# Kernel optimization log

Measured on AMD Instinct MI355X. Metric: run time of the kernel, lower is better.

The kernel has to match this reference:

```python
import jax, jax.numpy as jnp
import numpy as np
from jax import lax

BN_EPS = 1e-5
HEADS = 2


def dw_conv(x, w, stride, pad):
    # depthwise conv, NCHW, weight OIHW with I=1, groups=C
    return lax.conv_general_dilated(
        x, w, (stride, stride), [(pad, pad), (pad, pad)],
        dimension_numbers=('NCHW', 'OIHW', 'NCHW'),
        feature_group_count=x.shape[1])


def bn(x, g, b, m, v):
    inv = g * lax.rsqrt(v + BN_EPS)
    return (x - m[:, None, None]) * inv[:, None, None] + b[:, None, None]


def conv1x1(x, w, b):
    return jnp.einsum('bchw,oc->bohw', x, w) + b[:, None, None]


def setup_inputs() -> dict:
    key = jax.random.key(0)
    ks = jax.random.split(key, 20)
    B, C, H, W = 32, 128, 56, 56
    r = lambda i, shape, s=0.05: jax.random.normal(ks[i], shape, jnp.float32) * s
    return {
        'x': jax.random.normal(ks[0], (B, C, H, W), jnp.float32),
        'q_w': r(1, (C, C)), 'q_b': r(2, (C,)),
        'kv_w': r(3, (2 * C, C)), 'kv_b': r(4, (2 * C,)),
        'sr1_w': r(5, (C, 1, 4, 4), 0.2),
        'sr1_g': jax.random.uniform(ks[6], (C,), jnp.float32) + 0.5,
        'sr1_b': r(7, (C,)),
        'sr1_m': r(8, (C,)),
        'sr1_v': jax.random.uniform(ks[9], (C,), jnp.float32) + 0.5,
        'sr2_w': r(10, (C, 1, 1, 1), 0.5),
        'sr2_g': jax.random.uniform(ks[11], (C,), jnp.float32) + 0.5,
        'sr2_b': r(12, (C,)),
        'sr2_m': r(13, (C,)),
        'sr2_v': jax.random.uniform(ks[14], (C,), jnp.float32) + 0.5,
        'local_w': r(15, (C, 1, 3, 3), 0.2), 'local_b': r(16, (C,)),
    }


def reference(x, q_w, q_b, kv_w, kv_b,
              sr1_w, sr1_g, sr1_b, sr1_m, sr1_v,
              sr2_w, sr2_g, sr2_b, sr2_m, sr2_v,
              local_w, local_b):
    B, C, H, W = x.shape
    h = HEADS
    d = C // h
    scale = d ** -0.5

    # q projection: 1x1 conv -> [B, h, N, d]
    q = conv1x1(x, q_w, q_b)
    q = q.reshape(B, h, d, H * W).transpose(0, 1, 3, 2)

    # spatial reduction: depthwise strided conv + BN + ReLU, then depthwise 1x1 + BN
    kv = jax.nn.relu(bn(dw_conv(x, sr1_w, 4, 2), sr1_g, sr1_b, sr1_m, sr1_v))
    kv = bn(kv * sr2_w.reshape(C, 1, 1), sr2_g, sr2_b, sr2_m, sr2_v)

    # depthwise 3x3 local conv + residual
    kv = dw_conv(kv, local_w, 1, 1) + local_b[:, None, None] + kv

    # kv projection and split
    kvp = conv1x1(kv, kv_w, kv_b)
    k, v = jnp.split(kvp, 2, axis=1)
    Nk = k.shape[2] * k.shape[3]
    k = k.reshape(B, h, d, Nk)                       # [B,h,d,Nk]
    v = v.reshape(B, h, d, Nk).transpose(0, 1, 3, 2)  # [B,h,Nk,d]

    attn = jax.nn.softmax(jnp.einsum('bhnd,bhdm->bhnm', q, k) * scale, axis=-1)
    out = jnp.einsum('bhnm,bhmd->bhnd', attn, v)      # [B,h,N,d]
    return out.transpose(0, 1, 3, 2).reshape(B, C, H, W)
```

## Files before the change

kernel.cpp:

```cpp
#include <hip/hip_runtime.h>
#include <hip/hip_bf16.h>

#define B_    32
#define C_    128
#define H_    56
#define W_    56
#define N_    3136
#define HK_   15
#define NK_   225
#define D_    64

typedef __attribute__((ext_vector_type(8))) short bf16x8;
typedef __attribute__((ext_vector_type(4))) float f32x4;

__device__ __forceinline__ float b2f(unsigned short u) {
    union { float f; unsigned int i; } x;
    x.i = ((unsigned int)u) << 16;
    return x.f;
}
__device__ __forceinline__ unsigned short f2b(float f) {
    __hip_bfloat16 h = __float2bfloat16(f);
    return *(unsigned short*)&h;
}

__device__ __forceinline__ void gll16(const char* g, char* l) {
    __builtin_amdgcn_global_load_lds(
        (const __attribute__((address_space(1))) unsigned int*)g,
        (__attribute__((address_space(3))) unsigned int*)l,
        16, 0, 0);
}

__global__ __launch_bounds__(256) void srlocal_kernel(
        const float* __restrict__ x,
        const float* __restrict__ sr1_w, const float* __restrict__ sr1_g,
        const float* __restrict__ sr1_b, const float* __restrict__ sr1_m,
        const float* __restrict__ sr1_v, const float* __restrict__ sr2_w,
        const float* __restrict__ sr2_g, const float* __restrict__ sr2_b,
        const float* __restrict__ sr2_m, const float* __restrict__ sr2_v,
        const float* __restrict__ local_w, const float* __restrict__ local_b,
        float* __restrict__ kv2) {
    int bc = blockIdx.x;
    int c  = bc & (C_ - 1);
    int tid = threadIdx.x;
    __shared__ float xim[H_ * W_];
    __shared__ float kvt[HK_][HK_ + 1];

    const float* xp = x + (size_t)bc * (H_ * W_);
    for (int idx = tid; idx < (H_ * W_) / 4; idx += 256)
        ((float4*)xim)[idx] = ((const float4*)xp)[idx];
    __syncthreads();

    int p = tid;
    int oy = p / HK_, ox = p % HK_;
    if (p < NK_) {
        float s = 0.f;
#pragma unroll
        for (int ky = 0; ky < 4; ++ky) {
            int iy = oy * 4 - 2 + ky;
            if (iy < 0 || iy >= H_) continue;
#pragma unroll
            for (int kx = 0; kx < 4; ++kx) {
                int ix = ox * 4 - 2 + kx;
                if (ix < 0 || ix >= W_) continue;
                s += xim[iy * W_ + ix] * sr1_w[c * 16 + ky * 4 + kx];
            }
        }
        float inv1 = sr1_g[c] * rsqrtf(sr1_v[c] + 1e-5f);
        s = (s - sr1_m[c]) * inv1 + sr1_b[c];
        s = fmaxf(s, 0.f);
        s *= sr2_w[c];
        float inv2 = sr2_g[c] * rsqrtf(sr2_v[c] + 1e-5f);
        s = (s - sr2_m[c]) * inv2 + sr2_b[c];
        kvt[oy][ox] = s;
    }
    __syncthreads();
    if (p < NK_) {
        float v = kvt[oy][ox] + local_b[c];
#pragma unroll
        for (int dy = -1; dy <= 1; ++dy) {
            int yy = oy + dy;
            if (yy < 0 || yy >= HK_) continue;
#pragma unroll
            for (int dx = -1; dx <= 1; ++dx) {
                int xx = ox + dx;
                if (xx < 0 || xx >= HK_) continue;
                v += kvt[yy][xx] * local_w[c * 9 + (dy + 1) * 3 + (dx + 1)];
            }
        }
        kv2[(size_t)bc * NK_ + p] = v;
    }
}

__global__ __launch_bounds__(256) void wprep_kernel(
        const float* __restrict__ q_w, const float* __restrict__ q_b,
        const float* __restrict__ kv_w, const float* __restrict__ kv_b,
        unsigned short* __restrict__ wkq_sw, unsigned short* __restrict__ wv_sw,
        float* __restrict__ kwb, float* __restrict__ wb, float* __restrict__ qkb) {
    int bx = blockIdx.x;
    int h  = bx >> 3, cg = bx & 7;
    int tid = threadIdx.x;
    __shared__ float wk_s[64][128];
    __shared__ float wq_s[64][16];

    for (int idx = tid; idx < 64 * 128; idx += 256)
        wk_s[idx >> 7][idx & 127] = kv_w[(size_t)(h * 64 + (idx >> 7)) * 128 + (idx & 127)];
    for (int idx = tid; idx < 64 * 16; idx += 256)
        wq_s[idx >> 4][idx & 15] = q_w[(size_t)(h * 64 + (idx >> 4)) * 128 + cg * 16 + (idx & 15)];
    __syncthreads();

    {
        int cl = tid >> 4;
        int c  = cg * 16 + cl;
        int cp0 = (tid & 15) * 8;
        float acc[8];
#pragma unroll
        for (int i = 0; i < 8; ++i) acc[i] = 0.f;
        for (int e = 0; e < 64; ++e) {
            float wqv = wq_s[e][cl];
#pragma unroll
            for (int i = 0; i < 8; ++i) acc[i] += wqv * wk_s[e][cp0 + i];
        }
        char* base = (char*)wkq_sw + (size_t)h * 32768 + (size_t)c * 256;
        ushort4 u0, u1;
        u0.x = f2b(acc[0] * 0.125f); u0.y = f2b(acc[1] * 0.125f);
        u0.z = f2b(acc[2] * 0.125f); u0.w = f2b(acc[3] * 0.125f);
        u1.x = f2b(acc[4] * 0.125f); u1.y = f2b(acc[5] * 0.125f);
        u1.z = f2b(acc[6] * 0.125f); u1.w = f2b(acc[7] * 0.125f);
        int sw = (c & 7) << 4;
        *(ushort4*)(base + ((cp0 * 2) ^ sw)) = u0;
        *(ushort4*)(base + ((cp0 * 2 + 8) ^ sw)) = u1;
    }
    if (tid < 16) {
        int cl = tid, c = cg * 16 + cl;
        float s = 0.f;
        for (int e = 0; e < 64; ++e) s += kv_b[h * 64 + e] * wq_s[e][cl];
        kwb[h * 128 + c] = s * 0.125f;
    }
    if (cg == 0) {
        if (tid < 128) {
            float s = 0.f;
            for (int e = 0; e < 64; ++e) s += q_b[h * 64 + e] * wk_s[e][tid];
            wb[h * 128 + tid] = s * 0.125f;
        }
        if (tid == 0) {
            float s = 0.f;
            for (int e = 0; e < 64; ++e) s += q_b[h * 64 + e] * kv_b[h * 64 + e];
            qkb[h] = s * 0.125f;
        }
    }
    if (cg == 1) {
        for (int idx = tid; idx < 64 * 128; idx += 256) {
            int e = idx >> 7, cp = idx & 127;
            unsigned short val = f2b(kv_w[(size_t)(128 + h * 64 + e) * 128 + cp]);
            *(unsigned short*)((char*)wv_sw + (size_t)h * 16384 + (size_t)e * 256 +
                               (((cp * 2) ^ ((e & 7) << 4)))) = val;
        }
    }
}

#define L2B(r, cb) ((r) * 256 + ((cb) ^ (((r) & 7) << 4)))
__global__ __launch_bounds__(256, 2) void kvw_kernel(
        const float* __restrict__ kv2,
        const float* __restrict__ kv_b,
        const unsigned short* __restrict__ wkq_sw,
        const unsigned short* __restrict__ wv_sw,
        const float* __restrict__ kwb,
        const float* __restrict__ wb,
        const float* __restrict__ qkb,
        unsigned short* __restrict__ kw,
        float* __restrict__ bias_s,
        unsigned short* __restrict__ vbuf) {
    int b = blockIdx.x, h = blockIdx.y, mh = blockIdx.z;
    int bh = b * 2 + h;
    int m0 = mh * 64;
    int tid = threadIdx.x;
    int lo = tid & 15, hi = (tid >> 4) & 3, wid = tid >> 6;

    __shared__ char K2[16384];
    __shared__ char WQ[32768];
    __shared__ char WV[16384];

    {
        const char* srcQ = (const char*)wkq_sw + (size_t)h * 32768 + tid * 16;
        char* dstQ = WQ + wid * 1024;
#pragma unroll
        for (int i = 0; i < 8; ++i) gll16(srcQ + i * 4096, dstQ + i * 4096);
        const char* srcV = (const char*)wv_sw + (size_t)h * 16384 + tid * 16;
        char* dstV = WV + wid * 1024;
#pragma unroll
        for (int i = 0; i < 4; ++i) gll16(srcV + i * 4096, dstV + i * 4096);
    }
    {
        int j = tid & 63;
        int mg = m0 + j;
        bool val = (mg < NK_);
#pragma unroll
        for (int it = 0; it < 8; ++it) {
            int c0 = (tid >> 6) * 4 + it * 16;
            ushort4 u;
            if (val) {
                const float* kp = kv2 + ((size_t)b * 128 + c0) * NK_ + mg;
                u.x = f2b(kp[0]);
                u.y = f2b(kp[NK_]);
                u.z = f2b(kp[2 * NK_]);
                u.w = f2b(kp[3 * NK_]);
            } else { u.x = 0; u.y = 0; u.z = 0; u.w = 0; }
            *(ushort4*)(K2 + L2B(j, c0 * 2)) = u;
        }
    }
    __syncthreads();

    bf16x8 aq[4];
#pragma unroll
    for (int ks = 0; ks < 4; ++ks)
        aq[ks] = *(const bf16x8*)(K2 + L2B(wid * 16 + lo, ks * 64 + hi * 16));

    char* kwB = (char*)kw + (size_t)bh * 65536;
#pragma unroll
    for (int ct = 0; ct < 8; ++ct) {
        f32x4 acc = {0.f, 0.f, 0.f, 0.f};
#pragma unroll
        for (int ks = 0; ks < 4; ++ks) {
            bf16x8 bq = *(const bf16x8*)(WQ + L2B(ct * 16 + lo, ks * 64 + hi * 16));
            acc = __builtin_amdgcn_mfma_f32_16x16x32_bf16(aq[ks], bq, acc, 0, 0, 0);
        }
        int c = ct * 16 + lo;
        float kb = kwb[h * 128 + c];
#pragma unroll
        for (int r = 0; r < 4; ++r) {
            int mg = m0 + wid * 16 + hi * 4 + r;
            *(unsigned short*)(kwB + (size_t)mg * 256 + (((c * 2) ^ ((mg & 7) << 4)))) =
                f2b(acc[r] + kb);
        }
    }

    char* vB = (char*)vbuf + (size_t)bh * 32768;
#pragma unroll
    for (int et = 0; et < 4; ++et) {
        f32x4 acc = {0.f, 0.f, 0.f, 0.f};
#pragma unroll
        for (int ks = 0; ks < 4; ++ks) {
            bf16x8 bv = *(const bf16x8*)(WV + L2B(et * 16 + lo, ks * 64 + hi * 16));
            acc = __builtin_amdgcn_mfma_f32_16x16x32_bf16(aq[ks], bv, acc, 0, 0, 0);
        }
        int e = et * 16 + lo;
        float vb = kv_b[128 + h * 64 + e];
#pragma unroll
        for (int r = 0; r < 4; ++r) {
            int mg = m0 + wid * 16 + hi * 4 + r;
            *(unsigned short*)(vB + (size_t)e * 512 + (((mg * 2) ^ ((e & 7) << 4)))) =
                f2b(acc[r] + vb);
        }
    }

    if (tid < 64) {
        int mg = m0 + tid;
        float s;
        if (mg >= NK_) s = -1e30f;
        else {
            s = qkb[h];
            for (int i = 0; i < 128; ++i) {
                int cp = (i + (tid & 7) * 16) & 127;
                s += b2f(*(const unsigned short*)(K2 + L2B(tid, cp * 2))) * wb[h * 128 + cp];
            }
        }
        bias_s[(size_t)bh * 256 + mg] = s;
    }
}

#define XTB(j, c) ((j) * 256 + (((c) * 2) ^ (((j) & 7) << 4)))
#define PSB(j, m) ((j) * 512 + (((m) * 2) ^ (((j) & 7) << 4)))
#define KWB(rl, cb) ((rl) * 256 + ((cb) ^ (((rl) & 7) << 4)))
#define CVB(e, cb)  ((e) * 512 + ((cb) ^ (((e) & 7) << 4)))

__global__ __launch_bounds__(256, 2) void attn_kernel(
        const float* __restrict__ x,
        const unsigned short* __restrict__ kw,
        const float* __restrict__ bias_s,
        const unsigned short* __restrict__ vbuf,
        float* __restrict__ out) {
    int jt = blockIdx.x;
    int h  = blockIdx.y;
    int bb = blockIdx.z;
    int n0 = jt * 64;
    int bh = bb * 2 + h;
    int tid = threadIdx.x;
    int lo  = tid & 15;
    int hi  = (tid >> 4) & 3;
    int wid = tid >> 6;
    int jw  = wid * 16;

    __shared__ char A[32768];
    __shared__ char Bt[12288];
    __shared__ char Cv[32768];

    const char* kwG = (const char*)kw + (size_t)bh * 65536;
    const char* vG  = (const char*)vbuf + (size_t)bh * 32768;

    float bs[15];
    const float* bsp = bias_s + (size_t)bh * 256;
#pragma unroll
    for (int mt = 0; mt < 15; ++mt) bs[mt] = bsp[mt * 16 + lo];

    {
        char* dstB = Bt + wid * 1024;
        const char* srcB = kwG + tid * 16;
#pragma unroll
        for (int i = 0; i < 3; ++i) gll16(srcB + i * 4096, dstB + i * 4096);
        char* dstC = Cv + wid * 1024;
        const char* srcC = vG + tid * 16;
#pragma unroll
        for (int i = 0; i < 8; ++i) gll16(srcC + i * 4096, dstC + i * 4096);
    }

#pragma unroll
    for (int it = 0; it < 8; ++it) {
        int j  = tid & 63;
        int c0 = (tid >> 6) * 4 + it * 16;
        const float* xp = x + ((size_t)bb * 128 + c0) * N_ + n0 + j;
        ushort4 u;
        u.x = f2b(xp[0]);
        u.y = f2b(xp[(size_t)N_]);
        u.z = f2b(xp[2 * (size_t)N_]);
        u.w = f2b(xp[3 * (size_t)N_]);
        *(ushort4*)(A + XTB(j, c0)) = u;
    }
    __syncthreads();

    bf16x8 aq[4];
#pragma unroll
    for (int ks = 0; ks < 4; ++ks)
        aq[ks] = *(const bf16x8*)(A + XTB(jw + lo, ks * 32 + hi * 8));

    f32x4 s[15];
#pragma unroll
    for (int t = 0; t < 5; ++t) {
#pragma unroll
        for (int ml = 0; ml < 3; ++ml) {
            f32x4 acc = {0.f, 0.f, 0.f, 0.f};
#pragma unroll
            for (int ks = 0; ks < 4; ++ks) {
                bf16x8 bk = *(const bf16x8*)(Bt + KWB(ml * 16 + lo, ks * 64 + hi * 16));
                acc = __builtin_amdgcn_mfma_f32_16x16x32_bf16(aq[ks], bk, acc, 0, 0, 0);
            }
            s[t * 3 + ml] = acc;
        }
        if (t < 4) {
            __syncthreads();
            const char* srcB = kwG + (t + 1) * 12288 + tid * 16;
            char* dstB = Bt + wid * 1024;
#pragma unroll
            for (int i = 0; i < 3; ++i) gll16(srcB + i * 4096, dstB + i * 4096);
            __syncthreads();
        }
    }

#pragma unroll
    for (int mt = 0; mt < 15; ++mt) {
#pragma unroll
        for (int r = 0; r < 4; ++r) s[mt][r] += bs[mt];
    }

    float mx[4];
#pragma unroll
    for (int r = 0; r < 4; ++r) {
        float m0v = s[0][r];
#pragma unroll
        for (int mt = 1; mt < 15; ++mt) m0v = fmaxf(m0v, s[mt][r]);
        mx[r] = m0v;
    }
#pragma unroll
    for (int d = 1; d < 16; d <<= 1) {
#pragma unroll
        for (int r = 0; r < 4; ++r) mx[r] = fmaxf(mx[r], __shfl_xor(mx[r], d));
    }
    float sm[4] = {0.f, 0.f, 0.f, 0.f};
#pragma unroll
    for (int mt = 0; mt < 15; ++mt) {
#pragma unroll
        for (int r = 0; r < 4; ++r) {
            float pe = __expf(s[mt][r] - mx[r]);
            s[mt][r] = pe;
            sm[r] += pe;
        }
    }
#pragma unroll
    for (int d = 1; d < 16; d <<= 1) {
#pragma unroll
        for (int r = 0; r < 4; ++r) sm[r] += __shfl_xor(sm[r], d);
    }
    float rinv[4];
#pragma unroll
    for (int r = 0; r < 4; ++r) rinv[r] = 1.f / sm[r];

#pragma unroll
    for (int mt = 0; mt < 15; ++mt) {
#pragma unroll
        for (int r = 0; r < 4; ++r)
            *(unsigned short*)(A + PSB(jw + hi * 4 + r, mt * 16 + lo)) =
                f2b(s[mt][r] * rinv[r]);
    }
#pragma unroll
    for (int r = 0; r < 4; ++r)
        *(unsigned short*)(A + PSB(jw + hi * 4 + r, 240 + lo)) = 0;

    bf16x8 bp[8];
#pragma unroll
    for (int ks = 0; ks < 8; ++ks)
        bp[ks] = *(const bf16x8*)(A + PSB(jw + lo, ks * 32 + hi * 8));
#pragma unroll
    for (int et = 0; et < 4; ++et) {
        f32x4 acc = {0.f, 0.f, 0.f, 0.f};
#pragma unroll
        for (int ks = 0; ks < 8; ++ks) {
            bf16x8 av = *(const bf16x8*)(Cv + CVB(et * 16 + lo, ks * 64 + hi * 16));
            acc = __builtin_amdgcn_mfma_f32_16x16x32_bf16(av, bp[ks], acc, 0, 0, 0);
        }
        int e = et * 16 + hi * 4;
#pragma unroll
        for (int r = 0; r < 4; ++r)
            out[((size_t)bb * 128 + h * 64 + e + r) * N_ + n0 + jw + lo] = acc[r];
    }
}

extern "C" void kernel_launch(void* const* d_in, const int* in_sizes, int n_in,
                              void* d_out, int out_size, void* d_ws, size_t ws_size,
                              hipStream_t stream) {
    const float* x       = (const float*)d_in[0];
    const float* q_w     = (const float*)d_in[1];
    const float* q_b     = (const float*)d_in[2];
    const float* kv_w    = (const float*)d_in[3];
    const float* kv_b    = (const float*)d_in[4];
    const float* sr1_w   = (const float*)d_in[5];
    const float* sr1_g   = (const float*)d_in[6];
    const float* sr1_b   = (const float*)d_in[7];
    const float* sr1_m   = (const float*)d_in[8];
    const float* sr1_v   = (const float*)d_in[9];
    const float* sr2_w   = (const float*)d_in[10];
    const float* sr2_g   = (const float*)d_in[11];
    const float* sr2_b   = (const float*)d_in[12];
    const float* sr2_m   = (const float*)d_in[13];
    const float* sr2_v   = (const float*)d_in[14];
    const float* local_w = (const float*)d_in[15];
    const float* local_b = (const float*)d_in[16];

    char* ws = (char*)d_ws;
    float* kv2              = (float*)(ws + 0);
    unsigned short* wkq_sw  = (unsigned short*)(ws + 3686400);
    unsigned short* wv_sw   = (unsigned short*)(ws + 3751936);
    unsigned short* kw      = (unsigned short*)(ws + 3784704);
    unsigned short* vbuf    = (unsigned short*)(ws + 7979008);
    float* bias_s           = (float*)(ws + 10076160);
    float* kwb              = (float*)(ws + 10141696);
    float* wb               = (float*)(ws + 10142720);
    float* qkb              = (float*)(ws + 10143744);

    wprep_kernel<<<16, 256, 0, stream>>>(q_w, q_b, kv_w, kv_b,
                                         wkq_sw, wv_sw, kwb, wb, qkb);
    srlocal_kernel<<<B_ * C_, 256, 0, stream>>>(
        x, sr1_w, sr1_g, sr1_b, sr1_m, sr1_v,
        sr2_w, sr2_g, sr2_b, sr2_m, sr2_v, local_w, local_b, kv2);
    kvw_kernel<<<dim3(B_, 2, 4), 256, 0, stream>>>(
        kv2, kv_b, wkq_sw, wv_sw, kwb, wb, qkb, kw, bias_s, vbuf);
    attn_kernel<<<dim3(49, 2, B_), 256, 0, stream>>>(
        x, kw, bias_s, vbuf, (float*)d_out);
}
```

Before: 105.6 us.

## Double-buffer key-weight tiles with fine-grained waitcnt barriers in attention kernel

Replaces the single 12KB key tile buffer, which needed two full syncthreads per step, with two 8KB ping-pong buffers. Prefetch is issued two steps ahead and gated by explicit vmcnt waits and raw s_barrier, so MFMA work overlaps the global-to-LDS loads. The softmax bias is staged through LDS, and the key loop now covers all 16 tiles, relying on -1e30 bias padding instead of explicit zero-filled probability columns. The XOR swizzle for the x/P tiles widens to 16 rows to reduce LDS bank conflicts. The hand-tuned waitcnt counts are fragile and add one extra tile of MFMA work.

```diff
diff --git a/kernel.cpp b/kernel.cpp
--- a/kernel.cpp
+++ b/kernel.cpp
@@ -268,8 +268,8 @@
     }
 }
 
-#define XTB(j, c) ((j) * 256 + (((c) * 2) ^ (((j) & 7) << 4)))
-#define PSB(j, m) ((j) * 512 + (((m) * 2) ^ (((j) & 7) << 4)))
+#define XTB(j, c) ((j) * 256 + (((c) * 2) ^ (((j) & 15) << 4)))
+#define PSB(j, m) ((j) * 512 + (((m) * 2) ^ (((j) & 15) << 4)))
 #define KWB(rl, cb) ((rl) * 256 + ((cb) ^ (((rl) & 7) << 4)))
 #define CVB(e, cb)  ((e) * 512 + ((cb) ^ (((e) & 7) << 4)))
 
@@ -291,27 +291,11 @@
     int jw  = wid * 16;
 
     __shared__ char A[32768];
-    __shared__ char Bt[12288];
+    __shared__ char Bt[2][8192];
     __shared__ char Cv[32768];
 
     const char* kwG = (const char*)kw + (size_t)bh * 65536;
     const char* vG  = (const char*)vbuf + (size_t)bh * 32768;
-
-    float bs[15];
-    const float* bsp = bias_s + (size_t)bh * 256;
-#pragma unroll
-    for (int mt = 0; mt < 15; ++mt) bs[mt] = bsp[mt * 16 + lo];
-
-    {
-        char* dstB = Bt + wid * 1024;
-        const char* srcB = kwG + tid * 16;
-#pragma unroll
-        for (int i = 0; i < 3; ++i) gll16(srcB + i * 4096, dstB + i * 4096);
-        char* dstC = Cv + wid * 1024;
-        const char* srcC = vG + tid * 16;
-#pragma unroll
-        for (int i = 0; i < 8; ++i) gll16(srcC + i * 4096, dstC + i * 4096);
-    }
 
 #pragma unroll
     for (int it = 0; it < 8; ++it) {
@@ -325,48 +309,78 @@
         u.w = f2b(xp[3 * (size_t)N_]);
         *(ushort4*)(A + XTB(j, c0)) = u;
     }
-    __syncthreads();
+    {
+        float bsl = bias_s[(size_t)bh * 256 + tid];
+        *(float*)(A + 16384 + tid * 4) = bsl;
+    }
+    {
+        const char* s0 = kwG + tid * 16;
+        char* d0 = Bt[0] + wid * 1024;
+        gll16(s0, d0); gll16(s0 + 4096, d0 + 4096);
+        const char* s1 = kwG + 8192 + tid * 16;
+        char* d1 = Bt[1] + wid * 1024;
+        gll16(s1, d1); gll16(s1 + 4096, d1 + 4096);
+        const char* sc = vG + tid * 16;
+        char* dc = Cv + wid * 1024;
+#pragma unroll
+        for (int i = 0; i < 8; ++i) gll16(sc + i * 4096, dc + i * 4096);
+    }
+    asm volatile("s_waitcnt vmcnt(10) lgkmcnt(0)" ::: "memory");
+    __builtin_amdgcn_s_barrier();
+    __builtin_amdgcn_sched_barrier(0);
 
     bf16x8 aq[4];
 #pragma unroll
     for (int ks = 0; ks < 4; ++ks)
         aq[ks] = *(const bf16x8*)(A + XTB(jw + lo, ks * 32 + hi * 8));
 
-    f32x4 s[15];
-#pragma unroll
-    for (int t = 0; t < 5; ++t) {
-#pragma unroll
-        for (int ml = 0; ml < 3; ++ml) {
+    f32x4 s[16];
+#pragma unroll
+    for (int t = 0; t < 8; ++t) {
+#pragma unroll
+        for (int ml = 0; ml < 2; ++ml) {
             f32x4 acc = {0.f, 0.f, 0.f, 0.f};
 #pragma unroll
             for (int ks = 0; ks < 4; ++ks) {
-                bf16x8 bk = *(const bf16x8*)(Bt + KWB(ml * 16 + lo, ks * 64 + hi * 16));
+                bf16x8 bk = *(const bf16x8*)(Bt[t & 1] + KWB(ml * 16 + lo, ks * 64 + hi * 16));
                 acc = __builtin_amdgcn_mfma_f32_16x16x32_bf16(aq[ks], bk, acc, 0, 0, 0);
             }
-            s[t * 3 + ml] = acc;
-        }
-        if (t < 4) {
-            __syncthreads();
-            const char* srcB = kwG + (t + 1) * 12288 + tid * 16;
-            char* dstB = Bt + wid * 1024;
-#pragma unroll
-            for (int i = 0; i < 3; ++i) gll16(srcB + i * 4096, dstB + i * 4096);
-            __syncthreads();
-        }
-    }
-
-#pragma unroll
-    for (int mt = 0; mt < 15; ++mt) {
+            s[t * 2 + ml] = acc;
+        }
+        if (t < 6) {
+            __builtin_amdgcn_s_barrier();
+            const char* sn = kwG + (t + 2) * 8192 + tid * 16;
+            char* dn = Bt[t & 1] + wid * 1024;
+            gll16(sn, dn); gll16(sn + 4096, dn + 4096);
+        }
+        if (t < 7) {
+            if (t == 0)      asm volatile("s_waitcnt vmcnt(10)" ::: "memory");
+            else if (t < 6)  asm volatile("s_waitcnt vmcnt(2)" ::: "memory");
+            else             asm volatile("s_waitcnt vmcnt(0)" ::: "memory");
+            __builtin_amdgcn_s_barrier();
+            __builtin_amdgcn_sched_barrier(0);
+        }
+    }
+
+    float bs[16];
+#pragma unroll
+    for (int mt = 0; mt < 16; ++mt)
+        bs[mt] = *(const float*)(A + 16384 + (mt * 16 + lo) * 4);
+#pragma unroll
+    for (int mt = 0; mt < 16; ++mt) {
 #pragma unroll
         for (int r = 0; r < 4; ++r) s[mt][r] += bs[mt];
     }
+    asm volatile("s_waitcnt lgkmcnt(0)" ::: "memory");
+    __builtin_amdgcn_s_barrier();
+    __builtin_amdgcn_sched_barrier(0);
 
     float mx[4];
 #pragma unroll
     for (int r = 0; r < 4; ++r) {
         float m0v = s[0][r];
 #pragma unroll
-        for (int mt = 1; mt < 15; ++mt) m0v = fmaxf(m0v, s[mt][r]);
+        for (int mt = 1; mt < 16; ++mt) m0v = fmaxf(m0v, s[mt][r]);
         mx[r] = m0v;
     }
 #pragma unroll
@@ -376,7 +390,7 @@
     }
     float sm[4] = {0.f, 0.f, 0.f, 0.f};
 #pragma unroll
-    for (int mt = 0; mt < 15; ++mt) {
+    for (int mt = 0; mt < 16; ++mt) {
 #pragma unroll
         for (int r = 0; r < 4; ++r) {
             float pe = __expf(s[mt][r] - mx[r]);
@@ -394,15 +408,12 @@
     for (int r = 0; r < 4; ++r) rinv[r] = 1.f / sm[r];
 
 #pragma unroll
-    for (int mt = 0; mt < 15; ++mt) {
+    for (int mt = 0; mt < 16; ++mt) {
 #pragma unroll
         for (int r = 0; r < 4; ++r)
             *(unsigned short*)(A + PSB(jw + hi * 4 + r, mt * 16 + lo)) =
                 f2b(s[mt][r] * rinv[r]);
     }
-#pragma unroll
-    for (int r = 0; r < 4; ++r)
-        *(unsigned short*)(A + PSB(jw + hi * 4 + r, 240 + lo)) = 0;
 
     bf16x8 bp[8];
 #pragma unroll
```

Measured after the change: 105.9 us. No clear change (+0.3%).
